# Optimization experiments

Hardware: AMD Instinct MI355X
Metric: run time of the kernel (lower is better)

Reference implementation:

```python
import jax, jax.numpy as jnp
import numpy as np

N = 8192        # num nodes
F_IN = 256      # input feature dim
HEADS = 4
HEAD_DIM = 64   # out_dim // heads = 256 // 4
NEG_SLOPE = 0.2 # standard GAT LeakyReLU slope


def setup_inputs() -> dict:
    key = jax.random.key(0)
    k1, k2, k3, k4, k5 = jax.random.split(key, 5)
    x = jax.random.normal(k1, (N, F_IN), dtype=jnp.float32)
    adj = jax.random.randint(k2, (N, N), 0, 2, dtype=jnp.int32)
    # glorot-uniform-ish scale for kernel
    lim = float(np.sqrt(6.0 / (F_IN + HEADS * HEAD_DIM)))
    W = jax.random.uniform(k3, (F_IN, HEADS, HEAD_DIM), dtype=jnp.float32, minval=-lim, maxval=lim)
    a_src = jax.random.normal(k4, (HEADS, HEAD_DIM), dtype=jnp.float32) * 0.1
    a_dst = jax.random.normal(k5, (HEADS, HEAD_DIM), dtype=jnp.float32) * 0.1
    bias = jnp.zeros((HEADS * HEAD_DIM,), dtype=jnp.float32)
    return {"x": x, "adj": adj, "W": W, "a_src": a_src, "a_dst": a_dst, "bias": bias}


def reference(x, adj, W, a_src, a_dst, bias):
    # per-head linear transform: [N, H, D]
    h = jnp.einsum('nf,fhd->nhd', x, W)
    # decomposed attention logits: e_ij = leaky_relu(a_src.h_i + a_dst.h_j)
    src = jnp.einsum('nhd,hd->nh', h, a_src)  # [N, H]
    dst = jnp.einsum('nhd,hd->nh', h, a_dst)  # [N, H]
    e = jax.nn.leaky_relu(src[:, None, :] + dst[None, :, :], NEG_SLOPE)  # [N, N, H]
    mask = adj[:, :, None] > 0
    e = jnp.where(mask, e, jnp.float32(-1e9))
    alpha = jax.nn.softmax(e, axis=1)  # softmax over neighbors j for each target i
    out = jnp.einsum('ijh,jhd->ihd', alpha, h)  # aggregate neighbor features
    return out.reshape(N, HEADS * HEAD_DIM) + bias  # concat heads + bias
```

## Files before the change

### kernel.cpp

```cpp
#include <hip/hip_runtime.h>
#include <cstdint>
#include <cstddef>

#define NN 8192
#define HEADS 4

typedef __attribute__((ext_vector_type(4))) float  f4;
typedef __attribute__((ext_vector_type(4))) int    i4;
typedef __attribute__((ext_vector_type(8))) short  short8;
typedef __attribute__((ext_vector_type(4))) unsigned int   u4;
typedef unsigned int   uint32;

__device__ __forceinline__ unsigned short f2bf(float f) {
    unsigned int u = __builtin_bit_cast(unsigned int, f);
    u += 0x7FFFu + ((u >> 16) & 1u);
    return (unsigned short)(u >> 16);
}

__global__ __launch_bounds__(256) void k0_convert(const float* __restrict__ W,
                                                  unsigned short* __restrict__ WT) {
    int f = blockIdx.x;
    int c = threadIdx.x;
    WT[c * 256 + f] = f2bf(W[f * 256 + c]);
}

__device__ __forceinline__ short8 ld8bf(const float* __restrict__ p) {
    f4 lo = *(const f4*)p;
    f4 hi = *(const f4*)(p + 4);
    short8 r;
    r[0] = f2bf(lo.x); r[1] = f2bf(lo.y); r[2] = f2bf(lo.z); r[3] = f2bf(lo.w);
    r[4] = f2bf(hi.x); r[5] = f2bf(hi.y); r[6] = f2bf(hi.z); r[7] = f2bf(hi.w);
    return r;
}

__global__ __launch_bounds__(256) void k1_hgemm(
    const float* __restrict__ x, const unsigned short* __restrict__ WT,
    const float* __restrict__ aS, const float* __restrict__ aD,
    unsigned short* __restrict__ hF,
    float* __restrict__ sE, float* __restrict__ sE2,
    float* __restrict__ dE, float* __restrict__ dE2)
{
    const int tid  = threadIdx.x;
    const int head = tid >> 6;
    const int lane = tid & 63;
    const int col  = lane & 15;
    const int quad = lane >> 4;
    const int i0   = blockIdx.x * 32;

    const float* ar0 = x + (size_t)(i0 + col) * 256 + quad * 8;
    const float* ar1 = ar0 + 16 * 256;
    const unsigned short* br = WT + (size_t)(head * 64 + col) * 256 + quad * 8;

    f4 C[2][4];
    #pragma unroll
    for (int a = 0; a < 2; a++)
        #pragma unroll
        for (int b = 0; b < 4; b++) C[a][b] = f4{0.f, 0.f, 0.f, 0.f};

    #pragma unroll
    for (int kk = 0; kk < 256; kk += 32) {
        short8 a0 = ld8bf(ar0 + kk);
        short8 a1 = ld8bf(ar1 + kk);
        #pragma unroll
        for (int nt = 0; nt < 4; nt++) {
            short8 bf = *(const short8*)(br + nt * 16 * 256 + kk);
            C[0][nt] = __builtin_amdgcn_mfma_f32_16x16x32_bf16(a0, bf, C[0][nt], 0, 0, 0);
            C[1][nt] = __builtin_amdgcn_mfma_f32_16x16x32_bf16(a1, bf, C[1][nt], 0, 0, 0);
        }
    }

    float as_[4], ad_[4];
    #pragma unroll
    for (int nt = 0; nt < 4; nt++) {
        as_[nt] = aS[head * 64 + nt * 16 + col];
        ad_[nt] = aD[head * 64 + nt * 16 + col];
    }
    #pragma unroll
    for (int mt = 0; mt < 2; mt++) {
        #pragma unroll
        for (int r = 0; r < 4; r++) {
            float sv = 0.f, dv = 0.f;
            #pragma unroll
            for (int nt = 0; nt < 4; nt++) {
                sv += C[mt][nt][r] * as_[nt];
                dv += C[mt][nt][r] * ad_[nt];
            }
            #pragma unroll
            for (int m = 1; m < 16; m <<= 1) {
                sv += __shfl_xor(sv, m, 64);
                dv += __shfl_xor(dv, m, 64);
            }
            if (col == 0) {
                int i = i0 + mt * 16 + quad * 4 + r;
                float zs = sv * 1.4426950408889634f;
                float zd = dv * 1.4426950408889634f;
                sE [head * NN + i] = __builtin_amdgcn_exp2f(zs);
                sE2[head * NN + i] = __builtin_amdgcn_exp2f(0.2f * zs);
                dE [head * NN + i] = __builtin_amdgcn_exp2f(zd);
                dE2[head * NN + i] = __builtin_amdgcn_exp2f(0.2f * zd);
            }
        }
    }

    const size_t fbase = (((size_t)blockIdx.x * HEADS + head) * 4) * 512;
    #pragma unroll
    for (int mt = 0; mt < 2; mt++) {
        #pragma unroll
        for (int nt = 0; nt < 4; nt++) {
            #pragma unroll
            for (int r = 0; r < 4; r++) {
                int il = mt * 16 + quad * 4 + r;
                int qp = il >> 3;
                int t  = il & 7;
                hF[fbase + (size_t)nt * 512 + (qp * 16 + col) * 8 + t] =
                    f2bf(C[mt][nt][r]);
            }
        }
    }
}

__device__ __forceinline__ short8 build_w(uint32 bits,
                                          const f4& alo, const f4& ahi,
                                          const f4& blo, const f4& bhi,
                                          float es, float es2) {
    float aa[8] = {alo[0], alo[1], alo[2], alo[3], ahi[0], ahi[1], ahi[2], ahi[3]};
    float bb[8] = {blo[0], blo[1], blo[2], blo[3], bhi[0], bhi[1], bhi[2], bhi[3]};
    float e[8];
    #pragma unroll
    for (int t = 0; t < 8; t++) {
        float av = es  * aa[t];
        float bv = es2 * bb[t];
        float m  = fmaxf(av, bv);
        float mf = (float)((bits >> t) & 1u);
        e[t] = m * mf;
    }
    u4 pv;
    #pragma unroll
    for (int t = 0; t < 4; t++) {
        uint32 e0 = __builtin_bit_cast(uint32, e[2 * t])     + 0x8000u;
        uint32 e1 = __builtin_bit_cast(uint32, e[2 * t + 1]) + 0x8000u;
        pv[t] = __builtin_amdgcn_perm(e1, e0, 0x07060302u);
    }
    return __builtin_bit_cast(short8, pv);
}

__global__ __launch_bounds__(256, 4) void k2_gat(
    const int* __restrict__ adj, const unsigned short* __restrict__ hF,
    const float* __restrict__ sE, const float* __restrict__ sE2,
    const float* __restrict__ dE, const float* __restrict__ dE2,
    float* __restrict__ Pout, float* __restrict__ PS,
    int jshift, int jchunk)
{
    const int tid   = threadIdx.x;
    const int head  = tid >> 6;
    const int lane  = tid & 63;
    const int col   = lane & 15;
    const int quad  = lane >> 4;
    const int split = blockIdx.x & ((1 << jshift) - 1);
    const int itile = blockIdx.x >> jshift;
    const int i0    = itile * 32;
    const int j0    = split * jchunk;

    __shared__ uint32 abits[2][32][4];

    const float es0  = sE [head * NN + i0 + col];
    const float es0b = sE2[head * NN + i0 + col];
    const float es1  = sE [head * NN + i0 + 16 + col];
    const float es1b = sE2[head * NN + i0 + 16 + col];

    const float* dEp  = dE  + head * NN + j0 + quad * 8;
    const float* dE2p = dE2 + head * NN + j0 + quad * 8;
    const unsigned short* hbase =
        hF + ((size_t)(j0 >> 5) * HEADS + head) * 4 * 512 + lane * 8;

    const int* abase = adj + (size_t)(i0 + head * 8) * NN + j0 + lane;

    f4 acc[2][4];
    f4 accS[2];
    #pragma unroll
    for (int a = 0; a < 2; a++) {
        accS[a] = f4{0.f, 0.f, 0.f, 0.f};
        #pragma unroll
        for (int b = 0; b < 4; b++) acc[a][b] = f4{0.f, 0.f, 0.f, 0.f};
    }
    short8 ones;
    #pragma unroll
    for (int t = 0; t < 8; t++) ones[t] = (short)0x3F80;

    const int ngrp = jchunk >> 7;

    int st[16];
    auto issue = [&](int g) {
        #pragma unroll
        for (int r = 0; r < 8; ++r) {
            const int* rp = abase + (size_t)r * NN + g * 128;
            st[2 * r]     = rp[0];
            st[2 * r + 1] = rp[64];
        }
    };
    auto commit = [&](int buf) {
        #pragma unroll
        for (int r = 0; r < 8; ++r) {
            unsigned long long m0 = __ballot(st[2 * r]     != 0);
            unsigned long long m1 = __ballot(st[2 * r + 1] != 0);
            if (lane == 0) {
                abits[buf][head * 8 + r][0] = (uint32)m0;
                abits[buf][head * 8 + r][1] = (uint32)(m0 >> 32);
                abits[buf][head * 8 + r][2] = (uint32)m1;
                abits[buf][head * 8 + r][3] = (uint32)(m1 >> 32);
            }
        }
    };

    issue(0);
    commit(0);
    __syncthreads();

    for (int g = 0; g < ngrp; ++g) {
        const int cur = g & 1;
        if (g + 1 < ngrp) issue(g + 1);

        #pragma unroll
        for (int k = 0; k < 4; ++k) {
            const int jb = g * 4 + k;
            const float* dp  = dEp  + jb * 32;
            const float* dp2 = dE2p + jb * 32;
            f4 alo = *(const f4*)(dp);
            f4 ahi = *(const f4*)(dp + 4);
            f4 blo = *(const f4*)(dp2);
            f4 bhi = *(const f4*)(dp2 + 4);
            const unsigned short* hp = hbase + (size_t)jb * (HEADS * 4 * 512);
            short8 B0 = *(const short8*)(hp);
            short8 B1 = *(const short8*)(hp + 512);
            short8 B2 = *(const short8*)(hp + 1024);
            short8 B3 = *(const short8*)(hp + 1536);

            uint32 w0 = abits[cur][col][k];
            uint32 w1 = abits[cur][col + 16][k];
            uint32 b0 = (w0 >> (quad * 8)) & 0xFFu;
            uint32 b1 = (w1 >> (quad * 8)) & 0xFFu;
            short8 af0 = build_w(b0, alo, ahi, blo, bhi, es0, es0b);
            short8 af1 = build_w(b1, alo, ahi, blo, bhi, es1, es1b);

            acc[0][0] = __builtin_amdgcn_mfma_f32_16x16x32_bf16(af0, B0, acc[0][0], 0, 0, 0);
            acc[0][1] = __builtin_amdgcn_mfma_f32_16x16x32_bf16(af0, B1, acc[0][1], 0, 0, 0);
            acc[0][2] = __builtin_amdgcn_mfma_f32_16x16x32_bf16(af0, B2, acc[0][2], 0, 0, 0);
            acc[0][3] = __builtin_amdgcn_mfma_f32_16x16x32_bf16(af0, B3, acc[0][3], 0, 0, 0);
            accS[0]   = __builtin_amdgcn_mfma_f32_16x16x32_bf16(af0, ones, accS[0], 0, 0, 0);
            acc[1][0] = __builtin_amdgcn_mfma_f32_16x16x32_bf16(af1, B0, acc[1][0], 0, 0, 0);
            acc[1][1] = __builtin_amdgcn_mfma_f32_16x16x32_bf16(af1, B1, acc[1][1], 0, 0, 0);
            acc[1][2] = __builtin_amdgcn_mfma_f32_16x16x32_bf16(af1, B2, acc[1][2], 0, 0, 0);
            acc[1][3] = __builtin_amdgcn_mfma_f32_16x16x32_bf16(af1, B3, acc[1][3], 0, 0, 0);
            accS[1]   = __builtin_amdgcn_mfma_f32_16x16x32_bf16(af1, ones, accS[1], 0, 0, 0);
        }

        if (g + 1 < ngrp) commit(cur ^ 1);
        __syncthreads();
    }

    #pragma unroll
    for (int mt = 0; mt < 2; mt++) {
        #pragma unroll
        for (int nt = 0; nt < 4; nt++) {
            #pragma unroll
            for (int r = 0; r < 4; r++) {
                int row = i0 + mt * 16 + quad * 4 + r;
                Pout[((size_t)split * NN + row) * 256 + head * 64 + nt * 16 + col] =
                    acc[mt][nt][r];
            }
        }
        if (col == 0) {
            #pragma unroll
            for (int r = 0; r < 4; r++) {
                int row = i0 + mt * 16 + quad * 4 + r;
                PS[((size_t)split * NN + row) * HEADS + head] = accS[mt][r];
            }
        }
    }
}

__global__ void k3_norm(const float* __restrict__ Pout, const float* __restrict__ PS,
                        const float* __restrict__ bias, float* __restrict__ out,
                        int jsplit)
{
    int t  = blockIdx.x * 256 + threadIdx.x;
    int c4 = t * 4;
    int i    = c4 >> 8;
    int cb   = c4 & 255;
    int head = cb >> 6;
    f4 num = f4{0.f, 0.f, 0.f, 0.f};
    float den = 0.f;
    for (int s = 0; s < jsplit; s++) {
        num += *(const f4*)(Pout + ((size_t)s * NN + i) * 256 + cb);
        den += PS[((size_t)s * NN + i) * HEADS + head];
    }
    f4 bv = *(const f4*)(bias + cb);
    f4 o  = num * (1.0f / den) + bv;
    *(f4*)(out + c4) = o;
}

extern "C" void kernel_launch(void* const* d_in, const int* in_sizes, int n_in,
                              void* d_out, int out_size, void* d_ws, size_t ws_size,
                              hipStream_t stream) {
    (void)in_sizes; (void)n_in; (void)out_size;
    const float* x    = (const float*)d_in[0];
    const int*   adj  = (const int*)d_in[1];
    const float* W    = (const float*)d_in[2];
    const float* aS   = (const float*)d_in[3];
    const float* aD   = (const float*)d_in[4];
    const float* bias = (const float*)d_in[5];
    float* out = (float*)d_out;

    char* ws = (char*)d_ws;
    unsigned short* WT = (unsigned short*)(ws);
    unsigned short* hF = (unsigned short*)(ws +   131072);
    float*  sE   = (float*)(ws +  4325376);
    float*  sE2  = (float*)(ws +  4456448);
    float*  dE   = (float*)(ws +  4587520);
    float*  dE2  = (float*)(ws +  4718592);
    float*  PS   = (float*)(ws +  4849664);
    float*  Pout = (float*)(ws +  5898240);

    const size_t need8 = 5898240ull + 8ull * 8388608ull;
    const int jsplit = (ws_size >= need8) ? 8 : 4;
    const int jshift = (jsplit == 8) ? 3 : 2;
    const int jchunk = NN / jsplit;

    k0_convert<<<256, 256, 0, stream>>>(W, WT);
    k1_hgemm<<<256, 256, 0, stream>>>(x, WT, aS, aD, hF, sE, sE2, dE, dE2);
    k2_gat<<<256 * jsplit, 256, 0, stream>>>(adj, hF, sE, sE2, dE, dE2, Pout, PS, jshift, jchunk);
    k3_norm<<<2048, 256, 0, stream>>>(Pout, PS, bias, out, jsplit);
}
```

Baseline: 438.8 us.

## Double GAT row tile to 64 to reuse h and dst loads across more rows

Each k2_gat block now covers 64 target rows instead of 32, running four M-subtiles per wave. The aim is to amortise the hF B-operand and dE/dE2 loads over twice as many MFMAs. The adjacency prefetch per wave doubles to 16 rows, and launch bounds drop to 2 waves/SIMD to make room for the extra accumulators and staging registers. In exchange the grid is halved, with fewer blocks and lower occupancy to hide adjacency load latency.

```diff
diff --git a/kernel.cpp b/kernel.cpp
--- a/kernel.cpp
+++ b/kernel.cpp
@@ -144,7 +144,7 @@
     return __builtin_bit_cast(short8, pv);
 }
 
-__global__ __launch_bounds__(256, 4) void k2_gat(
+__global__ __launch_bounds__(256, 2) void k2_gat(
     const int* __restrict__ adj, const unsigned short* __restrict__ hF,
     const float* __restrict__ sE, const float* __restrict__ sE2,
     const float* __restrict__ dE, const float* __restrict__ dE2,
@@ -158,27 +158,29 @@
     const int quad  = lane >> 4;
     const int split = blockIdx.x & ((1 << jshift) - 1);
     const int itile = blockIdx.x >> jshift;
-    const int i0    = itile * 32;
+    const int i0    = itile * 64;
     const int j0    = split * jchunk;
 
-    __shared__ uint32 abits[2][32][4];
-
-    const float es0  = sE [head * NN + i0 + col];
-    const float es0b = sE2[head * NN + i0 + col];
-    const float es1  = sE [head * NN + i0 + 16 + col];
-    const float es1b = sE2[head * NN + i0 + 16 + col];
+    __shared__ uint32 abits[2][64][4];
+
+    float es_[4], esb_[4];
+    #pragma unroll
+    for (int mt = 0; mt < 4; mt++) {
+        es_[mt]  = sE [head * NN + i0 + mt * 16 + col];
+        esb_[mt] = sE2[head * NN + i0 + mt * 16 + col];
+    }
 
     const float* dEp  = dE  + head * NN + j0 + quad * 8;
     const float* dE2p = dE2 + head * NN + j0 + quad * 8;
     const unsigned short* hbase =
         hF + ((size_t)(j0 >> 5) * HEADS + head) * 4 * 512 + lane * 8;
 
-    const int* abase = adj + (size_t)(i0 + head * 8) * NN + j0 + lane;
-
-    f4 acc[2][4];
-    f4 accS[2];
-    #pragma unroll
-    for (int a = 0; a < 2; a++) {
+    const int* abase = adj + (size_t)(i0 + head * 16) * NN + j0 + lane;
+
+    f4 acc[4][4];
+    f4 accS[4];
+    #pragma unroll
+    for (int a = 0; a < 4; a++) {
         accS[a] = f4{0.f, 0.f, 0.f, 0.f};
         #pragma unroll
         for (int b = 0; b < 4; b++) acc[a][b] = f4{0.f, 0.f, 0.f, 0.f};
@@ -189,10 +191,10 @@
 
     const int ngrp = jchunk >> 7;
 
-    int st[16];
+    int st[32];
     auto issue = [&](int g) {
         #pragma unroll
-        for (int r = 0; r < 8; ++r) {
+        for (int r = 0; r < 16; ++r) {
             const int* rp = abase + (size_t)r * NN + g * 128;
             st[2 * r]     = rp[0];
             st[2 * r + 1] = rp[64];
@@ -200,14 +202,14 @@
     };
     auto commit = [&](int buf) {
         #pragma unroll
-        for (int r = 0; r < 8; ++r) {
+        for (int r = 0; r < 16; ++r) {
             unsigned long long m0 = __ballot(st[2 * r]     != 0);
             unsigned long long m1 = __ballot(st[2 * r + 1] != 0);
             if (lane == 0) {
-                abits[buf][head * 8 + r][0] = (uint32)m0;
-                abits[buf][head * 8 + r][1] = (uint32)(m0 >> 32);
-                abits[buf][head * 8 + r][2] = (uint32)m1;
-                abits[buf][head * 8 + r][3] = (uint32)(m1 >> 32);
+                abits[buf][head * 16 + r][0] = (uint32)m0;
+                abits[buf][head * 16 + r][1] = (uint32)(m0 >> 32);
+                abits[buf][head * 16 + r][2] = (uint32)m1;
+                abits[buf][head * 16 + r][3] = (uint32)(m1 >> 32);
             }
         }
     };
@@ -235,23 +237,17 @@
             short8 B2 = *(const short8*)(hp + 1024);
             short8 B3 = *(const short8*)(hp + 1536);
 
-            uint32 w0 = abits[cur][col][k];
-            uint32 w1 = abits[cur][col + 16][k];
-            uint32 b0 = (w0 >> (quad * 8)) & 0xFFu;
-            uint32 b1 = (w1 >> (quad * 8)) & 0xFFu;
-            short8 af0 = build_w(b0, alo, ahi, blo, bhi, es0, es0b);
-            short8 af1 = build_w(b1, alo, ahi, blo, bhi, es1, es1b);
-
-            acc[0][0] = __builtin_amdgcn_mfma_f32_16x16x32_bf16(af0, B0, acc[0][0], 0, 0, 0);
-            acc[0][1] = __builtin_amdgcn_mfma_f32_16x16x32_bf16(af0, B1, acc[0][1], 0, 0, 0);
-            acc[0][2] = __builtin_amdgcn_mfma_f32_16x16x32_bf16(af0, B2, acc[0][2], 0, 0, 0);
-            acc[0][3] = __builtin_amdgcn_mfma_f32_16x16x32_bf16(af0, B3, acc[0][3], 0, 0, 0);
-            accS[0]   = __builtin_amdgcn_mfma_f32_16x16x32_bf16(af0, ones, accS[0], 0, 0, 0);
-            acc[1][0] = __builtin_amdgcn_mfma_f32_16x16x32_bf16(af1, B0, acc[1][0], 0, 0, 0);
-            acc[1][1] = __builtin_amdgcn_mfma_f32_16x16x32_bf16(af1, B1, acc[1][1], 0, 0, 0);
-            acc[1][2] = __builtin_amdgcn_mfma_f32_16x16x32_bf16(af1, B2, acc[1][2], 0, 0, 0);
-            acc[1][3] = __builtin_amdgcn_mfma_f32_16x16x32_bf16(af1, B3, acc[1][3], 0, 0, 0);
-            accS[1]   = __builtin_amdgcn_mfma_f32_16x16x32_bf16(af1, ones, accS[1], 0, 0, 0);
+            #pragma unroll
+            for (int mt = 0; mt < 4; mt++) {
+                uint32 w = abits[cur][mt * 16 + col][k];
+                uint32 b = (w >> (quad * 8)) & 0xFFu;
+                short8 af = build_w(b, alo, ahi, blo, bhi, es_[mt], esb_[mt]);
+                acc[mt][0] = __builtin_amdgcn_mfma_f32_16x16x32_bf16(af, B0, acc[mt][0], 0, 0, 0);
+                acc[mt][1] = __builtin_amdgcn_mfma_f32_16x16x32_bf16(af, B1, acc[mt][1], 0, 0, 0);
+                acc[mt][2] = __builtin_amdgcn_mfma_f32_16x16x32_bf16(af, B2, acc[mt][2], 0, 0, 0);
+                acc[mt][3] = __builtin_amdgcn_mfma_f32_16x16x32_bf16(af, B3, acc[mt][3], 0, 0, 0);
+                accS[mt]   = __builtin_amdgcn_mfma_f32_16x16x32_bf16(af, ones, accS[mt], 0, 0, 0);
+            }
         }
 
         if (g + 1 < ngrp) commit(cur ^ 1);
@@ -259,7 +255,7 @@
     }
 
     #pragma unroll
-    for (int mt = 0; mt < 2; mt++) {
+    for (int mt = 0; mt < 4; mt++) {
         #pragma unroll
         for (int nt = 0; nt < 4; nt++) {
             #pragma unroll
@@ -328,6 +324,6 @@
 
     k0_convert<<<256, 256, 0, stream>>>(W, WT);
     k1_hgemm<<<256, 256, 0, stream>>>(x, WT, aS, aD, hF, sE, sE2, dE, dE2);
-    k2_gat<<<256 * jsplit, 256, 0, stream>>>(adj, hF, sE, sE2, dE, dE2, Pout, PS, jshift, jchunk);
+    k2_gat<<<128 * jsplit, 256, 0, stream>>>(adj, hF, sE, sE2, dE, dE2, Pout, PS, jshift, jchunk);
     k3_norm<<<2048, 256, 0, stream>>>(Pout, PS, bias, out, jsplit);
 }
```

New measurement: 449.3 us. +2.4%, slower.

## Prefetch h feature tiles into LDS via async global_load_lds double buffering

Applied to the files above, without the earlier changes.

The per-j-block h fragments (B operands) are now copied one block ahead into a double-buffered LDS array with global_load_lds, instead of being loaded straight from global memory into registers right before the MFMAs. The adjacency prefetch moves inside the k loop, and explicit vmcnt waits with sched_barriers order the loads. The goal is to hide global load latency behind the MFMA work. The cost is extra LDS use (about 32KB per block), which may lower occupancy. The hand-counted vmcnt thresholds are fragile: each wave loads only its own head's slice and reads it back without a barrier, so a wrong count would read stale data.

```diff
diff --git a/kernel.cpp b/kernel.cpp
--- a/kernel.cpp
+++ b/kernel.cpp
@@ -162,6 +162,7 @@
     const int j0    = split * jchunk;
 
     __shared__ uint32 abits[2][32][4];
+    __shared__ __align__(16) unsigned short bfB[2][HEADS][2048];
 
     const float es0  = sE [head * NN + i0 + col];
     const float es0b = sE2[head * NN + i0 + col];
@@ -188,6 +189,7 @@
     for (int t = 0; t < 8; t++) ones[t] = (short)0x3F80;
 
     const int ngrp = jchunk >> 7;
+    const int njb  = jchunk >> 5;
 
     int st[16];
     auto issue = [&](int g) {
@@ -211,32 +213,55 @@
             }
         }
     };
-
+    auto issueB = [&](int jb, int buf) {
+        const unsigned short* hp = hbase + (size_t)jb * (HEADS * 4 * 512);
+        #pragma unroll
+        for (int f = 0; f < 4; ++f) {
+            __builtin_amdgcn_global_load_lds(
+                (const void*)(hp + f * 512),
+                (void*)&bfB[buf][head][f * 512], 16, 0, 0);
+        }
+    };
+
+    issueB(0, 0);
     issue(0);
     commit(0);
     __syncthreads();
 
     for (int g = 0; g < ngrp; ++g) {
-        const int cur = g & 1;
-        if (g + 1 < ngrp) issue(g + 1);
-
+        const int curg = g & 1;
+        const bool lastg = (g == ngrp - 1);
         #pragma unroll
         for (int k = 0; k < 4; ++k) {
             const int jb = g * 4 + k;
+            const int cb = jb & 1;
             const float* dp  = dEp  + jb * 32;
             const float* dp2 = dE2p + jb * 32;
             f4 alo = *(const f4*)(dp);
             f4 ahi = *(const f4*)(dp + 4);
             f4 blo = *(const f4*)(dp2);
             f4 bhi = *(const f4*)(dp2 + 4);
-            const unsigned short* hp = hbase + (size_t)jb * (HEADS * 4 * 512);
-            short8 B0 = *(const short8*)(hp);
-            short8 B1 = *(const short8*)(hp + 512);
-            short8 B2 = *(const short8*)(hp + 1024);
-            short8 B3 = *(const short8*)(hp + 1536);
-
-            uint32 w0 = abits[cur][col][k];
-            uint32 w1 = abits[cur][col + 16][k];
+            __builtin_amdgcn_sched_barrier(0);
+            if (jb + 1 < njb) issueB(jb + 1, cb ^ 1);
+            __builtin_amdgcn_sched_barrier(0);
+            if (k == 0 && g + 1 < ngrp) issue(g + 1);
+            __builtin_amdgcn_sched_barrier(0);
+            if (lastg) {
+                asm volatile("s_waitcnt vmcnt(0)" ::: "memory");
+            } else if (k <= 1) {
+                asm volatile("s_waitcnt vmcnt(24)" ::: "memory");
+            } else {
+                asm volatile("s_waitcnt vmcnt(8)" ::: "memory");
+            }
+            __builtin_amdgcn_sched_barrier(0);
+            const unsigned short* lb = &bfB[cb][head][lane * 8];
+            short8 B0 = *(const short8*)(lb);
+            short8 B1 = *(const short8*)(lb + 512);
+            short8 B2 = *(const short8*)(lb + 1024);
+            short8 B3 = *(const short8*)(lb + 1536);
+
+            uint32 w0 = abits[curg][col][k];
+            uint32 w1 = abits[curg][col + 16][k];
             uint32 b0 = (w0 >> (quad * 8)) & 0xFFu;
             uint32 b1 = (w1 >> (quad * 8)) & 0xFFu;
             short8 af0 = build_w(b0, alo, ahi, blo, bhi, es0, es0b);
@@ -254,7 +279,7 @@
             accS[1]   = __builtin_amdgcn_mfma_f32_16x16x32_bf16(af1, ones, accS[1], 0, 0, 0);
         }
 
-        if (g + 1 < ngrp) commit(cur ^ 1);
+        if (g + 1 < ngrp) commit(curg ^ 1);
         __syncthreads();
     }
 
```

Result: no change. 435.1 us (-0.9%).
